# Kernel tuning notes

Hardware: AMD Instinct MI355X
Metric: run time of the kernel (lower is better)

## Reference

```python
import jax, jax.numpy as jnp
import numpy as np

N, E, F_IN, HID, HEADS = 50000, 800000, 128, 64, 4


def setup_inputs() -> dict:
    key = jax.random.key(0)
    ks = jax.random.split(key, 10)
    def nrm(k, shape, scale=0.05):
        return jax.random.normal(k, shape, dtype=jnp.float32) * scale
    return {
        "x": jax.random.normal(ks[0], (N, F_IN), dtype=jnp.float32),
        "edge_index": jax.random.randint(ks[1], (2, E), 0, N),
        "W1": nrm(ks[2], (F_IN, HEADS * HID)),
        "att_src1": nrm(ks[3], (HEADS, HID)),
        "att_dst1": nrm(ks[4], (HEADS, HID)),
        "b1": jnp.zeros((HEADS * HID,), jnp.float32),
        "W2": nrm(ks[5], (HEADS * HID, HID)),
        "att_src2": nrm(ks[6], (1, HID)),
        "att_dst2": nrm(ks[7], (1, HID)),
        "b2": jnp.zeros((HID,), jnp.float32),
        "Wc": nrm(ks[8], (HID, 2)),
        "bc": jnp.zeros((2,), jnp.float32),
    }


def _segment_softmax(scores, seg, num_segments):
    # scores: [E, H]; softmax over all edges sharing the same dst node
    m = jax.ops.segment_max(scores, seg, num_segments=num_segments)
    m = jnp.where(jnp.isfinite(m), m, 0.0)  # nodes with no in-edges
    e = jnp.exp(scores - m[seg])
    s = jax.ops.segment_sum(e, seg, num_segments=num_segments)
    return e / (s[seg] + 1e-16)


def _gat_layer(x, src, dst, W, a_src, a_dst, b):
    # PyG GATConv (concat=True): h = xW -> [N,H,C]; alpha_ij = softmax_i(leaky_relu(a_s.h_j + a_d.h_i))
    n_nodes = x.shape[0]
    H, C = a_src.shape
    h = (x @ W).reshape(n_nodes, H, C)
    s_src = jnp.einsum('nhc,hc->nh', h, a_src)  # [N,H]
    s_dst = jnp.einsum('nhc,hc->nh', h, a_dst)  # [N,H]
    e = jax.nn.leaky_relu(s_src[src] + s_dst[dst], 0.2)  # [E,H]
    alpha = _segment_softmax(e, dst, n_nodes)            # [E,H]
    msg = h[src] * alpha[:, :, None]                     # [E,H,C] gather+weight
    out = jax.ops.segment_sum(msg, dst, num_segments=n_nodes)  # scatter-add
    return out.reshape(n_nodes, H * C) + b


def reference(x, edge_index, W1, att_src1, att_dst1, b1, W2, att_src2, att_dst2, b2, Wc, bc):
    n_nodes = x.shape[0]
    loops = jnp.arange(n_nodes)  # add_self_loops=True (PyG default)
    src = jnp.concatenate([edge_index[0], loops])
    dst = jnp.concatenate([edge_index[1], loops])
    # dropout layers are identity in eval mode
    h = _gat_layer(x, src, dst, W1, att_src1, att_dst1, b1)
    h = jax.nn.elu(h)
    h = _gat_layer(h, src, dst, W2, att_src2, att_dst2, b2)
    return h @ Wc + bc
```

## Files before the change

### kernel.cpp

```cpp
#include <hip/hip_runtime.h>
#include <hip/hip_fp16.h>
#include <math.h>

#define F_IN 128
#define C1 256
#define NH1 4
#define C2 64
#define CSH 4

typedef __attribute__((ext_vector_type(8))) _Float16 f16x8;
typedef __attribute__((ext_vector_type(4))) float f32x4;
typedef __attribute__((ext_vector_type(2))) float f32x2;

__device__ __forceinline__ float lrelu(float x) { return x >= 0.f ? x : 0.2f * x; }
__device__ __forceinline__ float elu(float x) { return x > 0.f ? x : expm1f(x); }
__device__ __forceinline__ int rli(int v, int j) { return __builtin_amdgcn_readlane(v, j); }

__device__ __forceinline__ void pkfma(f32x2& acc, f32x2 a, f32x2 b) {
    asm("v_pk_fma_f32 %0, %1, %2, %0" : "+v"(acc) : "v"(a), "v"(b));
}

struct __align__(8) H4 { __half2 a, b; };

__global__ __launch_bounds__(256) void k_init(int* __restrict__ cnt, int N, int zBlocks,
                                              const float* __restrict__ W1,
                                              const float* __restrict__ aS1,
                                              const float* __restrict__ aD1,
                                              float* __restrict__ atS,
                                              float* __restrict__ atD) {
    if ((int)blockIdx.x < zBlocks) {
        int i = blockIdx.x * 256 + threadIdx.x;
        if (i < N) cnt[(size_t)i << CSH] = 1;
    } else {
        int t3 = (blockIdx.x - zBlocks) * 256 + threadIdx.x;
        if (t3 < 1024) {
            bool isD = t3 >= 512;
            int r = t3 & 511;
            int h = r >> 7, k = r & 127;
            const float* a = isD ? aD1 : aS1;
            float s = 0.f;
            for (int c = 0; c < 64; ++c) s += W1[(size_t)k * C1 + h * 64 + c] * a[h * 64 + c];
            (isD ? atD : atS)[h * 128 + k] = s;
        }
    }
}

__global__ __launch_bounds__(256) void k_edges_prep(
    const int* __restrict__ esrc, const int* __restrict__ edst,
    int* __restrict__ cnt, int* __restrict__ elist, int E, int N,
    int countBlocks, int prepBlocks,
    const float* __restrict__ W1, const float* __restrict__ W2,
    __half* __restrict__ W1T, __half* __restrict__ W2T,
    const float* __restrict__ x, const float* __restrict__ atS,
    const float* __restrict__ atD, __half* __restrict__ xh,
    float* __restrict__ sS, float* __restrict__ sD) {
    int b = blockIdx.x;
    if (b < countBlocks) {
        int base = b * 4096 + threadIdx.x;
        int sv[16], dv[16], pv[16];
#pragma unroll
        for (int k = 0; k < 16; ++k) {
            int e = base + k * 256;
            int ss = 0, dd = -1;
            if (e < E) { ss = esrc[e]; dd = edst[e]; }
            sv[k] = ss; dv[k] = dd;
        }
#pragma unroll
        for (int k = 0; k < 8; ++k)
            pv[k] = (dv[k] >= 0) ? atomicAdd(&cnt[(size_t)dv[k] << CSH], 1) : 64;
#pragma unroll
        for (int k = 8; k < 16; ++k)
            pv[k] = (dv[k] >= 0) ? atomicAdd(&cnt[(size_t)dv[k] << CSH], 1) : 64;
#pragma unroll
        for (int k = 0; k < 8; ++k)
            if (dv[k] >= 0 && pv[k] < 64) elist[(dv[k] << 6) + pv[k]] = sv[k];
#pragma unroll
        for (int k = 8; k < 16; ++k)
            if (dv[k] >= 0 && pv[k] < 64) elist[(dv[k] << 6) + pv[k]] = sv[k];
    } else if (b < countBlocks + prepBlocks) {
        int tid = (b - countBlocks) * 256 + threadIdx.x;
        if (tid < F_IN * C1) {
            int k = tid >> 8, n = tid & 255;
            W1T[n * F_IN + k] = __float2half(W1[tid]);
        }
        int t2 = tid - F_IN * C1;
        if (t2 >= 0 && t2 < C1 * C2) {
            int k = t2 >> 6, n = t2 & 63;
            W2T[n * C1 + k] = __float2half(W2[t2]);
        }
    } else {
        int n = (b - countBlocks - prepBlocks) * 4 + (threadIdx.x >> 6);
        if (n >= N) return;
        int l = threadIdx.x & 63;
        float2 xv = *(const float2*)(x + (size_t)n * F_IN + l * 2);
        *(__half2*)(xh + (size_t)n * F_IN + l * 2) = __floats2half2_rn(xv.x, xv.y);
        float p[8];
#pragma unroll
        for (int h = 0; h < 4; ++h) {
            float2 a = *(const float2*)(atS + h * 128 + l * 2);
            float2 bb = *(const float2*)(atD + h * 128 + l * 2);
            p[h]     = xv.x * a.x + xv.y * a.y;
            p[4 + h] = xv.x * bb.x + xv.y * bb.y;
        }
#pragma unroll
        for (int off = 1; off < 64; off <<= 1) {
#pragma unroll
            for (int j = 0; j < 8; ++j) p[j] += __shfl_xor(p[j], off, 64);
        }
        if (l == 0) {
            *(float4*)(sS + n * 4) = make_float4(p[0], p[1], p[2], p[3]);
            *(float4*)(sD + n * 4) = make_float4(p[4], p[5], p[6], p[7]);
        }
    }
}

__global__ __launch_bounds__(256) void k_aggr1(const int* __restrict__ elist,
                                               const int* __restrict__ cnt,
                                               const float* __restrict__ sS,
                                               const float* __restrict__ sD,
                                               const __half* __restrict__ xh,
                                               __half* __restrict__ agg, int N) {
    __shared__ __align__(16) float wA[4][64][8];
    int wv = threadIdx.x >> 6, l = threadIdx.x & 63;
    int d = blockIdx.x * 4 + wv;
    if (d >= N) return;
    int len = cnt[(size_t)d << CSH]; if (len > 64) len = 64;
    int base = d << 6;
    float4 sd4 = *(const float4*)(sD + d * 4);
    const __half* xb = xh + l * 2;
    f32x2 a0 = {0.f, 0.f}, a1 = {0.f, 0.f}, a2 = {0.f, 0.f}, a3 = {0.f, 0.f};
    float4 den = {0.f, 0.f, 0.f, 0.f};
    int sl = 0;
    float4 w = {0.f, 0.f, 0.f, 0.f};
    if (l < len) {
        sl = (l == 0) ? d : elist[base + l];
        float4 s4 = *(const float4*)(sS + sl * 4);
        w.x = __expf(lrelu(s4.x + sd4.x));
        w.y = __expf(lrelu(s4.y + sd4.y));
        w.z = __expf(lrelu(s4.z + sd4.z));
        w.w = __expf(lrelu(s4.w + sd4.w));
        den.x = w.x; den.y = w.y; den.z = w.z; den.w = w.w;
    }
    *(float4*)&wA[wv][l][0] = make_float4(w.x, w.x, w.y, w.y);
    *(float4*)&wA[wv][l][4] = make_float4(w.z, w.z, w.w, w.w);
    __builtin_amdgcn_wave_barrier();
    int jm = (len + 3) & ~3;
    for (int j = 0; j < jm; j += 4) {
#pragma unroll
        for (int u = 0; u < 4; ++u) {
            int s = rli(sl, j + u);
            f32x4 q0 = *(const f32x4*)&wA[wv][j + u][0];
            f32x4 q1 = *(const f32x4*)&wA[wv][j + u][4];
            float2 f = __half22float2(*(const __half2*)(xb + ((size_t)(unsigned)s << 7)));
            f32x2 fv = {f.x, f.y};
            pkfma(a0, fv, f32x2{q0[0], q0[1]});
            pkfma(a1, fv, f32x2{q0[2], q0[3]});
            pkfma(a2, fv, f32x2{q1[0], q1[1]});
            pkfma(a3, fv, f32x2{q1[2], q1[3]});
        }
    }
#pragma unroll
    for (int off = 1; off < 64; off <<= 1) {
        den.x += __shfl_xor(den.x, off, 64);
        den.y += __shfl_xor(den.y, off, 64);
        den.z += __shfl_xor(den.z, off, 64);
        den.w += __shfl_xor(den.w, off, 64);
    }
    float i0 = 1.f / (den.x + 1e-16f), i1 = 1.f / (den.y + 1e-16f);
    float i2 = 1.f / (den.z + 1e-16f), i3 = 1.f / (den.w + 1e-16f);
    __half2* ag = (__half2*)(agg + (size_t)d * 512);
    ag[0 * 64 + l] = __floats2half2_rn(a0[0] * i0, a0[1] * i0);
    ag[1 * 64 + l] = __floats2half2_rn(a1[0] * i1, a1[1] * i1);
    ag[2 * 64 + l] = __floats2half2_rn(a2[0] * i2, a2[1] * i2);
    ag[3 * 64 + l] = __floats2half2_rn(a3[0] * i3, a3[1] * i3);
}

__global__ __launch_bounds__(256) void k_gemm12(
    const __half* __restrict__ agg, const __half* __restrict__ W1T,
    const float* __restrict__ b1, const __half* __restrict__ W2T,
    const float* __restrict__ aS, const float* __restrict__ aD,
    __half* __restrict__ h2h, float* __restrict__ sS, float* __restrict__ sD, int N) {
    __shared__ __align__(16) char smem[65536];
    __half* As  = (__half*)smem;
    __half* Bs1 = (__half*)(smem + 16384);
    __half* Bs2 = (__half*)smem;
    __half* o1L = (__half*)(smem + 32768);
    int t = threadIdx.x;
    int rowBase = blockIdx.x * 64;
    int lane = t & 63, wv = t >> 6;
    int lm = lane & 15, lk = lane >> 4;
    int rA = wv * 16 + lm;
    int row = rowBase + rA;

    for (int h = 0; h < 4; ++h) {
        __syncthreads();
        {
            int r = t >> 2;
            const uint4* src = (const uint4*)(agg + (size_t)(rowBase + r) * 512 + h * 128);
#pragma unroll
            for (int j = 0; j < 4; ++j) {
                int g = (t & 3) * 4 + j;
                uint4 v = {0, 0, 0, 0};
                if (rowBase + r < N) v = src[g];
                *(uint4*)&As[r * 128 + (g ^ (r & 7)) * 8] = v;
            }
        }
        {
            int r = t >> 2;
            const uint4* src = (const uint4*)(W1T + (size_t)(h * 64 + r) * 128);
#pragma unroll
            for (int j = 0; j < 4; ++j) {
                int g = (t & 3) * 4 + j;
                *(uint4*)&Bs1[r * 128 + (g ^ (r & 7)) * 8] = src[g];
            }
        }
        __syncthreads();
        f32x4 acc[4];
#pragma unroll
        for (int nt = 0; nt < 4; ++nt) acc[nt] = f32x4{0.f, 0.f, 0.f, 0.f};
#pragma unroll
        for (int kt = 0; kt < 4; ++kt) {
            int gs = ((kt * 4 + lk) ^ (lm & 7)) * 8;
            f16x8 af = *(const f16x8*)&As[rA * 128 + gs];
#pragma unroll
            for (int nt = 0; nt < 4; ++nt) {
                f16x8 bf = *(const f16x8*)&Bs1[(nt * 16 + lm) * 128 + gs];
                acc[nt] = __builtin_amdgcn_mfma_f32_16x16x32_f16(bf, af, acc[nt], 0, 0, 0);
            }
        }
#pragma unroll
        for (int nt = 0; nt < 4; ++nt) {
            int c = h * 64 + nt * 16 + lk * 4;
            float4 bb = *(const float4*)(b1 + c);
            H4 hv;
            hv.a = __floats2half2_rn(elu(acc[nt][0] + bb.x), elu(acc[nt][1] + bb.y));
            hv.b = __floats2half2_rn(elu(acc[nt][2] + bb.z), elu(acc[nt][3] + bb.w));
            int g = c >> 3;
            int gs2 = (g & ~7) | ((g & 7) ^ (rA & 7));
            *(H4*)((char*)o1L + rA * 512 + gs2 * 16 + (c & 7) * 2) = hv;
        }
    }
    __syncthreads();
    {
        int n = t & 63, gb = (t >> 6) * 8;
        const uint4* src = (const uint4*)(W2T + (size_t)n * C1);
#pragma unroll
        for (int j = 0; j < 8; ++j) {
            int g = gb + j;
            int gs = (g & ~7) | ((g & 7) ^ (n & 7));
            *(uint4*)&Bs2[n * 256 + gs * 8] = src[g];
        }
    }
    __syncthreads();

    f32x4 acc2[4];
#pragma unroll
    for (int nt = 0; nt < 4; ++nt) acc2[nt] = f32x4{0.f, 0.f, 0.f, 0.f};
#pragma unroll
    for (int kt2 = 0; kt2 < 8; ++kt2) {
        int g = kt2 * 4 + lk;
        int gs = (g & ~7) | ((g & 7) ^ (lm & 7));
        f16x8 af = *(const f16x8*)&o1L[rA * 256 + gs * 8];
#pragma unroll
        for (int nt = 0; nt < 4; ++nt) {
            f16x8 bf = *(const f16x8*)&Bs2[(nt * 16 + lm) * 256 + gs * 8];
            acc2[nt] = __builtin_amdgcn_mfma_f32_16x16x32_f16(bf, af, acc2[nt], 0, 0, 0);
        }
    }
    float ps = 0.f, pd = 0.f;
#pragma unroll
    for (int nt = 0; nt < 4; ++nt) {
        int cbase = nt * 16 + lk * 4;
        float a0 = acc2[nt][0], a1 = acc2[nt][1], a2 = acc2[nt][2], a3 = acc2[nt][3];
        float4 s4 = *(const float4*)(aS + cbase);
        float4 d4 = *(const float4*)(aD + cbase);
        ps += a0 * s4.x + a1 * s4.y + a2 * s4.z + a3 * s4.w;
        pd += a0 * d4.x + a1 * d4.y + a2 * d4.z + a3 * d4.w;
        if (row < N) {
            H4 hv;
            hv.a = __floats2half2_rn(a0, a1);
            hv.b = __floats2half2_rn(a2, a3);
            *(H4*)(h2h + (size_t)row * C2 + cbase) = hv;
        }
    }
    ps += __shfl_xor(ps, 16, 64); ps += __shfl_xor(ps, 32, 64);
    pd += __shfl_xor(pd, 16, 64); pd += __shfl_xor(pd, 32, 64);
    if (lk == 0 && row < N) { sS[row] = ps; sD[row] = pd; }
}

__global__ __launch_bounds__(256) void k_aggr2(const int* __restrict__ elist,
                                               const int* __restrict__ cnt,
                                               const float* __restrict__ sS,
                                               const float* __restrict__ sD,
                                               const __half* __restrict__ h2h,
                                               const float* __restrict__ b2,
                                               const float* __restrict__ Wc,
                                               const float* __restrict__ bc,
                                               float* __restrict__ out, int N) {
    __shared__ int sw[4][64][4];
    int wv = threadIdx.x >> 6, l = threadIdx.x & 63;
    int d = blockIdx.x * 4 + wv;
    if (d >= N) return;
    int half = l >> 5, c2 = l & 31;
    float sdd = sD[d];
    int len = cnt[(size_t)d << CSH]; if (len > 64) len = 64;
    int base = d << 6;
    f32x2 acc = {0.f, 0.f};
    float den = 0.f;
    const __half* hb = h2h + c2 * 2;
    int sl = 0; float w = 0.f;
    if (l < len) {
        sl = (l == 0) ? d : elist[base + l];
        w = __expf(lrelu(sS[sl] + sdd));
        den = w;
    }
    int4 e;
    e.x = sl; e.y = 0;
    e.z = __float_as_int(w); e.w = e.z;
    *(int4*)&sw[wv][l][0] = e;
    __builtin_amdgcn_wave_barrier();
    int pm = (len + 1) >> 1;
    int jm = (pm + 3) & ~3;
    for (int j = 0; j < jm; j += 4) {
        int4 q[4];
#pragma unroll
        for (int u = 0; u < 4; ++u)
            q[u] = *(const int4*)&sw[wv][2 * (j + u) + half][0];
        uint raw[4];
#pragma unroll
        for (int u = 0; u < 4; ++u)
            raw[u] = *(const uint*)(hb + ((size_t)(unsigned)q[u].x << 6));
#pragma unroll
        for (int u = 0; u < 4; ++u) {
            f32x2 wp = {__int_as_float(q[u].z), __int_as_float(q[u].w)};
            float2 f = __half22float2(*(__half2*)&raw[u]);
            pkfma(acc, f32x2{f.x, f.y}, wp);
        }
    }
#pragma unroll
    for (int off = 1; off < 64; off <<= 1) den += __shfl_xor(den, off, 64);
    float ax = acc[0], ay = acc[1];
    ax += __shfl_xor(ax, 32, 64);
    ay += __shfl_xor(ay, 32, 64);
    float inv = 1.f / (den + 1e-16f);
    float vx = ax * inv + b2[c2 * 2];
    float vy = ay * inv + b2[c2 * 2 + 1];
    float4 wc = *(const float4*)(Wc + c2 * 4);
    float p0 = vx * wc.x + vy * wc.z;
    float p1 = vx * wc.y + vy * wc.w;
    for (int off = 16; off; off >>= 1) {
        p0 += __shfl_down(p0, off, 32);
        p1 += __shfl_down(p1, off, 32);
    }
    if (l == 0) { out[d * 2 + 0] = p0 + bc[0]; out[d * 2 + 1] = p1 + bc[1]; }
}

extern "C" void kernel_launch(void* const* d_in, const int* in_sizes, int n_in,
                              void* d_out, int out_size, void* d_ws, size_t ws_size,
                              hipStream_t stream) {
    const float* x   = (const float*)d_in[0];
    const int*   ei  = (const int*)d_in[1];
    const float* W1  = (const float*)d_in[2];
    const float* aS1 = (const float*)d_in[3];
    const float* aD1 = (const float*)d_in[4];
    const float* b1  = (const float*)d_in[5];
    const float* W2  = (const float*)d_in[6];
    const float* aS2 = (const float*)d_in[7];
    const float* aD2 = (const float*)d_in[8];
    const float* b2  = (const float*)d_in[9];
    const float* Wc  = (const float*)d_in[10];
    const float* bc  = (const float*)d_in[11];
    float* out = (float*)d_out;

    int N = in_sizes[0] / F_IN;
    int E = in_sizes[1] / 2;
    const int* esrc = ei;
    const int* edst = ei + E;

    char* p = (char*)d_ws;
    __half* agg  = (__half*)p; p += (size_t)N * 512 * sizeof(__half);
    __half* xh   = (__half*)p; p += (size_t)N * F_IN * sizeof(__half);
    __half* h2h  = (__half*)p; p += (size_t)N * C2 * sizeof(__half);
    float* s1S   = (float*)p;  p += (size_t)N * NH1 * sizeof(float);
    float* s1D   = (float*)p;  p += (size_t)N * NH1 * sizeof(float);
    __half* W1T  = (__half*)p; p += (size_t)C1 * F_IN * sizeof(__half);
    __half* W2T  = (__half*)p; p += (size_t)C2 * C1 * sizeof(__half);
    float* atS   = (float*)p;  p += 512 * sizeof(float);
    float* atD   = (float*)p;  p += 512 * sizeof(float);
    float* s2S   = (float*)p;  p += (size_t)N * sizeof(float);
    float* s2D   = (float*)p;  p += (size_t)N * sizeof(float);
    int* cnt     = (int*)p;    p += ((size_t)N << CSH) * sizeof(int);
    int* elist   = (int*)p;    p += (size_t)N * 64 * sizeof(int);

    int zBlocks     = (N + 255) / 256;
    int countBlocks = (E + 4095) / 4096;
    int prepBlocks  = (F_IN * C1 + C1 * C2) / 256;
    int xprepBlocks = (N + 3) / 4;

    k_init<<<zBlocks + 4, 256, 0, stream>>>(cnt, N, zBlocks, W1, aS1, aD1, atS, atD);
    k_edges_prep<<<countBlocks + prepBlocks + xprepBlocks, 256, 0, stream>>>(
        esrc, edst, cnt, elist, E, N, countBlocks, prepBlocks,
        W1, W2, W1T, W2T, x, atS, atD, xh, s1S, s1D);

    k_aggr1<<<(N + 3) / 4, 256, 0, stream>>>(elist, cnt, s1S, s1D, xh, agg, N);
    k_gemm12<<<(N + 63) / 64, 256, 0, stream>>>(agg, W1T, b1, W2T, aS2, aD2, h2h, s2S, s2D, N);
    k_aggr2<<<(N + 3) / 4, 256, 0, stream>>>(elist, cnt, s2S, s2D, h2h, b2, Wc, bc, out, N);
}
```

Measured before the change: 171.7 us.

## Fold classifier into layer-2 GEMM so second aggregation gathers 2 floats

The final linear classifier Wc is pushed through the layer-2 softmax aggregation by linearity. The GEMM epilogue now projects each node's layer-2 features to two values (z2), and the second aggregation only gathers and weights those two floats per edge instead of 64 half values. Bias terms are folded into a constant computed once in k_init. The count array is now zeroed with hipMemsetAsync, and the self-loop slot is handled by offsetting edge-list writes by one. Rounding order changes slightly, and the fp16 storage of h2 is no longer used.

```diff
diff --git a/kernel.cpp b/kernel.cpp
--- a/kernel.cpp
+++ b/kernel.cpp
@@ -22,26 +22,29 @@
 
 struct __align__(8) H4 { __half2 a, b; };
 
-__global__ __launch_bounds__(256) void k_init(int* __restrict__ cnt, int N, int zBlocks,
-                                              const float* __restrict__ W1,
+__global__ __launch_bounds__(256) void k_init(const float* __restrict__ W1,
                                               const float* __restrict__ aS1,
                                               const float* __restrict__ aD1,
+                                              const float* __restrict__ b2,
+                                              const float* __restrict__ Wc,
+                                              const float* __restrict__ bc,
                                               float* __restrict__ atS,
-                                              float* __restrict__ atD) {
-    if ((int)blockIdx.x < zBlocks) {
-        int i = blockIdx.x * 256 + threadIdx.x;
-        if (i < N) cnt[(size_t)i << CSH] = 1;
-    } else {
-        int t3 = (blockIdx.x - zBlocks) * 256 + threadIdx.x;
-        if (t3 < 1024) {
-            bool isD = t3 >= 512;
-            int r = t3 & 511;
-            int h = r >> 7, k = r & 127;
-            const float* a = isD ? aD1 : aS1;
-            float s = 0.f;
-            for (int c = 0; c < 64; ++c) s += W1[(size_t)k * C1 + h * 64 + c] * a[h * 64 + c];
-            (isD ? atD : atS)[h * 128 + k] = s;
-        }
+                                              float* __restrict__ atD,
+                                              float* __restrict__ cW) {
+    if (blockIdx.x < 4) {
+        int t3 = blockIdx.x * 256 + threadIdx.x;
+        bool isD = t3 >= 512;
+        int r = t3 & 511;
+        int h = r >> 7, k = r & 127;
+        const float* a = isD ? aD1 : aS1;
+        float s = 0.f;
+        for (int c = 0; c < 64; ++c) s += W1[(size_t)k * C1 + h * 64 + c] * a[h * 64 + c];
+        (isD ? atD : atS)[h * 128 + k] = s;
+    } else if (threadIdx.x < 2) {
+        int j = threadIdx.x;
+        float s = bc[j];
+        for (int c = 0; c < 64; ++c) s += b2[c] * Wc[c * 2 + j];
+        cW[j] = s;
     }
 }
 
@@ -67,16 +70,16 @@
         }
 #pragma unroll
         for (int k = 0; k < 8; ++k)
-            pv[k] = (dv[k] >= 0) ? atomicAdd(&cnt[(size_t)dv[k] << CSH], 1) : 64;
+            pv[k] = (dv[k] >= 0) ? atomicAdd(&cnt[(size_t)dv[k] << CSH], 1) : 63;
 #pragma unroll
         for (int k = 8; k < 16; ++k)
-            pv[k] = (dv[k] >= 0) ? atomicAdd(&cnt[(size_t)dv[k] << CSH], 1) : 64;
+            pv[k] = (dv[k] >= 0) ? atomicAdd(&cnt[(size_t)dv[k] << CSH], 1) : 63;
 #pragma unroll
         for (int k = 0; k < 8; ++k)
-            if (dv[k] >= 0 && pv[k] < 64) elist[(dv[k] << 6) + pv[k]] = sv[k];
+            if (dv[k] >= 0 && pv[k] < 63) elist[(dv[k] << 6) + pv[k] + 1] = sv[k];
 #pragma unroll
         for (int k = 8; k < 16; ++k)
-            if (dv[k] >= 0 && pv[k] < 64) elist[(dv[k] << 6) + pv[k]] = sv[k];
+            if (dv[k] >= 0 && pv[k] < 63) elist[(dv[k] << 6) + pv[k] + 1] = sv[k];
     } else if (b < countBlocks + prepBlocks) {
         int tid = (b - countBlocks) * 256 + threadIdx.x;
         if (tid < F_IN * C1) {
@@ -124,7 +127,7 @@
     int wv = threadIdx.x >> 6, l = threadIdx.x & 63;
     int d = blockIdx.x * 4 + wv;
     if (d >= N) return;
-    int len = cnt[(size_t)d << CSH]; if (len > 64) len = 64;
+    int len = cnt[(size_t)d << CSH] + 1; if (len > 64) len = 64;
     int base = d << 6;
     float4 sd4 = *(const float4*)(sD + d * 4);
     const __half* xb = xh + l * 2;
@@ -179,7 +182,8 @@
     const __half* __restrict__ agg, const __half* __restrict__ W1T,
     const float* __restrict__ b1, const __half* __restrict__ W2T,
     const float* __restrict__ aS, const float* __restrict__ aD,
-    __half* __restrict__ h2h, float* __restrict__ sS, float* __restrict__ sD, int N) {
+    const float* __restrict__ Wc,
+    float* __restrict__ z2, float* __restrict__ sS, float* __restrict__ sD, int N) {
     __shared__ __align__(16) char smem[65536];
     __half* As  = (__half*)smem;
     __half* Bs1 = (__half*)(smem + 16384);
@@ -267,7 +271,7 @@
             acc2[nt] = __builtin_amdgcn_mfma_f32_16x16x32_f16(bf, af, acc2[nt], 0, 0, 0);
         }
     }
-    float ps = 0.f, pd = 0.f;
+    float ps = 0.f, pd = 0.f, z0 = 0.f, z1 = 0.f;
 #pragma unroll
     for (int nt = 0; nt < 4; ++nt) {
         int cbase = nt * 16 + lk * 4;
@@ -276,83 +280,51 @@
         float4 d4 = *(const float4*)(aD + cbase);
         ps += a0 * s4.x + a1 * s4.y + a2 * s4.z + a3 * s4.w;
         pd += a0 * d4.x + a1 * d4.y + a2 * d4.z + a3 * d4.w;
-        if (row < N) {
-            H4 hv;
-            hv.a = __floats2half2_rn(a0, a1);
-            hv.b = __floats2half2_rn(a2, a3);
-            *(H4*)(h2h + (size_t)row * C2 + cbase) = hv;
-        }
+        float4 w0 = *(const float4*)(Wc + cbase * 2);
+        float4 w1 = *(const float4*)(Wc + cbase * 2 + 4);
+        z0 += a0 * w0.x + a1 * w0.z + a2 * w1.x + a3 * w1.z;
+        z1 += a0 * w0.y + a1 * w0.w + a2 * w1.y + a3 * w1.w;
     }
     ps += __shfl_xor(ps, 16, 64); ps += __shfl_xor(ps, 32, 64);
     pd += __shfl_xor(pd, 16, 64); pd += __shfl_xor(pd, 32, 64);
-    if (lk == 0 && row < N) { sS[row] = ps; sD[row] = pd; }
+    z0 += __shfl_xor(z0, 16, 64); z0 += __shfl_xor(z0, 32, 64);
+    z1 += __shfl_xor(z1, 16, 64); z1 += __shfl_xor(z1, 32, 64);
+    if (lk == 0 && row < N) {
+        sS[row] = ps; sD[row] = pd;
+        *(float2*)(z2 + 2 * row) = make_float2(z0, z1);
+    }
 }
 
 __global__ __launch_bounds__(256) void k_aggr2(const int* __restrict__ elist,
                                                const int* __restrict__ cnt,
                                                const float* __restrict__ sS,
                                                const float* __restrict__ sD,
-                                               const __half* __restrict__ h2h,
-                                               const float* __restrict__ b2,
-                                               const float* __restrict__ Wc,
-                                               const float* __restrict__ bc,
+                                               const float* __restrict__ z2,
+                                               const float* __restrict__ cW,
                                                float* __restrict__ out, int N) {
-    __shared__ int sw[4][64][4];
     int wv = threadIdx.x >> 6, l = threadIdx.x & 63;
     int d = blockIdx.x * 4 + wv;
     if (d >= N) return;
-    int half = l >> 5, c2 = l & 31;
+    int len = cnt[(size_t)d << CSH] + 1; if (len > 64) len = 64;
     float sdd = sD[d];
-    int len = cnt[(size_t)d << CSH]; if (len > 64) len = 64;
-    int base = d << 6;
-    f32x2 acc = {0.f, 0.f};
-    float den = 0.f;
-    const __half* hb = h2h + c2 * 2;
-    int sl = 0; float w = 0.f;
+    float den = 0.f, nx = 0.f, ny = 0.f;
     if (l < len) {
-        sl = (l == 0) ? d : elist[base + l];
-        w = __expf(lrelu(sS[sl] + sdd));
-        den = w;
-    }
-    int4 e;
-    e.x = sl; e.y = 0;
-    e.z = __float_as_int(w); e.w = e.z;
-    *(int4*)&sw[wv][l][0] = e;
-    __builtin_amdgcn_wave_barrier();
-    int pm = (len + 1) >> 1;
-    int jm = (pm + 3) & ~3;
-    for (int j = 0; j < jm; j += 4) {
-        int4 q[4];
-#pragma unroll
-        for (int u = 0; u < 4; ++u)
-            q[u] = *(const int4*)&sw[wv][2 * (j + u) + half][0];
-        uint raw[4];
-#pragma unroll
-        for (int u = 0; u < 4; ++u)
-            raw[u] = *(const uint*)(hb + ((size_t)(unsigned)q[u].x << 6));
-#pragma unroll
-        for (int u = 0; u < 4; ++u) {
-            f32x2 wp = {__int_as_float(q[u].z), __int_as_float(q[u].w)};
-            float2 f = __half22float2(*(__half2*)&raw[u]);
-            pkfma(acc, f32x2{f.x, f.y}, wp);
-        }
-    }
-#pragma unroll
-    for (int off = 1; off < 64; off <<= 1) den += __shfl_xor(den, off, 64);
-    float ax = acc[0], ay = acc[1];
-    ax += __shfl_xor(ax, 32, 64);
-    ay += __shfl_xor(ay, 32, 64);
-    float inv = 1.f / (den + 1e-16f);
-    float vx = ax * inv + b2[c2 * 2];
-    float vy = ay * inv + b2[c2 * 2 + 1];
-    float4 wc = *(const float4*)(Wc + c2 * 4);
-    float p0 = vx * wc.x + vy * wc.z;
-    float p1 = vx * wc.y + vy * wc.w;
-    for (int off = 16; off; off >>= 1) {
-        p0 += __shfl_down(p0, off, 32);
-        p1 += __shfl_down(p1, off, 32);
-    }
-    if (l == 0) { out[d * 2 + 0] = p0 + bc[0]; out[d * 2 + 1] = p1 + bc[1]; }
+        int sl = (l == 0) ? d : elist[(d << 6) + l];
+        float2 z = *(const float2*)(z2 + 2 * sl);
+        float w = __expf(lrelu(sS[sl] + sdd));
+        den = w; nx = w * z.x; ny = w * z.y;
+    }
+#pragma unroll
+    for (int off = 1; off < 64; off <<= 1) {
+        den += __shfl_xor(den, off, 64);
+        nx  += __shfl_xor(nx,  off, 64);
+        ny  += __shfl_xor(ny,  off, 64);
+    }
+    if (l == 0) {
+        float inv = 1.f / (den + 1e-16f);
+        out[d * 2 + 0] = nx * inv + cW[0];
+        out[d * 2 + 1] = ny * inv + cW[1];
+    }
 }
 
 extern "C" void kernel_launch(void* const* d_in, const int* in_sizes, int n_in,
@@ -380,29 +352,30 @@
     char* p = (char*)d_ws;
     __half* agg  = (__half*)p; p += (size_t)N * 512 * sizeof(__half);
     __half* xh   = (__half*)p; p += (size_t)N * F_IN * sizeof(__half);
-    __half* h2h  = (__half*)p; p += (size_t)N * C2 * sizeof(__half);
+    float* z2    = (float*)p;  p += (size_t)N * 2 * sizeof(float);
     float* s1S   = (float*)p;  p += (size_t)N * NH1 * sizeof(float);
     float* s1D   = (float*)p;  p += (size_t)N * NH1 * sizeof(float);
     __half* W1T  = (__half*)p; p += (size_t)C1 * F_IN * sizeof(__half);
     __half* W2T  = (__half*)p; p += (size_t)C2 * C1 * sizeof(__half);
     float* atS   = (float*)p;  p += 512 * sizeof(float);
     float* atD   = (float*)p;  p += 512 * sizeof(float);
+    float* cW    = (float*)p;  p += 2 * sizeof(float);
     float* s2S   = (float*)p;  p += (size_t)N * sizeof(float);
     float* s2D   = (float*)p;  p += (size_t)N * sizeof(float);
     int* cnt     = (int*)p;    p += ((size_t)N << CSH) * sizeof(int);
     int* elist   = (int*)p;    p += (size_t)N * 64 * sizeof(int);
 
-    int zBlocks     = (N + 255) / 256;
     int countBlocks = (E + 4095) / 4096;
     int prepBlocks  = (F_IN * C1 + C1 * C2) / 256;
     int xprepBlocks = (N + 3) / 4;
 
-    k_init<<<zBlocks + 4, 256, 0, stream>>>(cnt, N, zBlocks, W1, aS1, aD1, atS, atD);
+    hipMemsetAsync(cnt, 0, ((size_t)N << CSH) * sizeof(int), stream);
+    k_init<<<5, 256, 0, stream>>>(W1, aS1, aD1, b2, Wc, bc, atS, atD, cW);
     k_edges_prep<<<countBlocks + prepBlocks + xprepBlocks, 256, 0, stream>>>(
         esrc, edst, cnt, elist, E, N, countBlocks, prepBlocks,
         W1, W2, W1T, W2T, x, atS, atD, xh, s1S, s1D);
 
     k_aggr1<<<(N + 3) / 4, 256, 0, stream>>>(elist, cnt, s1S, s1D, xh, agg, N);
-    k_gemm12<<<(N + 63) / 64, 256, 0, stream>>>(agg, W1T, b1, W2T, aS2, aD2, h2h, s2S, s2D, N);
-    k_aggr2<<<(N + 3) / 4, 256, 0, stream>>>(elist, cnt, s2S, s2D, h2h, b2, Wc, bc, out, N);
-}
+    k_gemm12<<<(N + 63) / 64, 256, 0, stream>>>(agg, W1T, b1, W2T, aS2, aD2, Wc, z2, s2S, s2D, N);
+    k_aggr2<<<(N + 3) / 4, 256, 0, stream>>>(elist, cnt, s2S, s2D, z2, cW, out, N);
+}
```

After: 167.9 us. 1.02x faster.
